# Optimization experiments

Measured on AMD Instinct MI355X. Metric: run time of the kernel, lower is better.

The kernel has to match this reference:

```python
import jax, jax.numpy as jnp
import numpy as np

N, E, D, H, OUT, L, AH = 50000, 800000, 128, 128, 2, 4, 16
LN_EPS = 1e-5


def setup_inputs() -> dict:
    key = jax.random.key(0)
    ks = jax.random.split(key, 8)
    s = lambda k, shape, scale: jax.random.normal(k, shape, jnp.float32) * scale
    return {
        "node_features": jax.random.normal(ks[0], (N, D), jnp.float32),
        "edge_index": jax.random.randint(ks[1], (2, E), 0, N),
        "W_self": s(ks[2], (L, D, H), 0.05),
        "b_self": jnp.zeros((L, H), jnp.float32),
        "W_ctx": s(ks[3], (L, 2 * D, H), 0.05),
        "b_ctx": jnp.zeros((L, H), jnp.float32),
        "att_W1": s(ks[4], (L, H, AH), 0.1),
        "att_b1": jnp.zeros((L, AH), jnp.float32),
        "att_w2": s(ks[5], (L, AH), 0.1),
        "ln_gamma": jnp.ones((L, H), jnp.float32),
        "ln_beta": jnp.zeros((L, H), jnp.float32),
        "fusion_logits": jnp.ones((L,), jnp.float32),
        "cls_W": s(ks[6], (H, OUT), 0.05),
        "cls_b": jnp.zeros((OUT,), jnp.float32),
    }


def _aggregate(x, src, tgt, n):
    # PyG add-aggregation of message cat([x_i - x_j, x_j]) at target nodes.
    # sum_over_edges(x_tgt - x_src) at tgt == deg(tgt)*x[tgt] - sum x_src, so we
    # avoid materializing the [E, 2D] edge tensor.
    ones = jnp.ones((src.shape[0],), x.dtype)
    deg = jax.ops.segment_sum(ones, tgt, num_segments=n)          # [N]
    agg_j = jax.ops.segment_sum(x[src], tgt, num_segments=n)      # [N, D]
    return jnp.concatenate([deg[:, None] * x - agg_j, agg_j], -1)  # [N, 2D]


def _layer_norm(x, gamma, beta):
    mu = x.mean(axis=-1, keepdims=True)
    var = ((x - mu) ** 2).mean(axis=-1, keepdims=True)
    return (x - mu) * jax.lax.rsqrt(var + LN_EPS) * gamma + beta


def _conv(x, src, tgt, Ws, bs, Wc, bc, A1, a1b, a2):
    n = x.shape[0]
    self_view = x @ Ws + bs                              # [N, H]
    out_view = _aggregate(x, src, tgt, n) @ Wc + bc      # outgoing (edge_index)
    in_view = _aggregate(x, tgt, src, n) @ Wc + bc       # incoming (reversed)
    mv = jnp.stack([self_view, out_view, in_view], axis=1)  # [N, 3, H]
    scores = jnp.einsum('nvh,ha->nva', jnp.tanh(jnp.einsum('nvh,ha->nva', mv, A1) + a1b), a2[:, None])[..., 0]
    w = jax.nn.softmax(scores, axis=1)                    # softmax over 3 views
    return jnp.einsum('nv,nvh->nh', w, mv)


def reference(node_features, edge_index, W_self, b_self, W_ctx, b_ctx,
              att_W1, att_b1, att_w2, ln_gamma, ln_beta,
              fusion_logits, cls_W, cls_b):
    src, tgt = edge_index[0], edge_index[1]
    x = node_features
    layer_outputs = []
    for l in range(L):
        h = _conv(x, src, tgt, W_self[l], b_self[l], W_ctx[l], b_ctx[l],
                  att_W1[l], att_b1[l], att_w2[l])
        h = jax.nn.relu(_layer_norm(h, ln_gamma[l], ln_beta[l]))
        # dropout is identity in eval mode
        x = h + x if l > 0 else h
        layer_outputs.append(x)
    fw = jax.nn.softmax(fusion_logits)
    fused = sum(fw[i] * layer_outputs[i] for i in range(L))
    return fused @ cls_W + cls_b
```

## Files before the change

kernel.cpp:

```cpp
#include <hip/hip_runtime.h>

#define N_NODES 50000
#define N_EDGES 800000
#define DD 128
#define HH 128
#define LL 4
#define AHH 16
#define LN_EPS 1e-5f
#define NCOLS 432
#define SCAN_B 512
#define SCAN_NB ((N_NODES + SCAN_B - 1) / SCAN_B)
#define WTPAD 136
#define WT_BLOCKS ((LL*NCOLS*DD)/256)
#define NBKT 196
#define BKT_CAP 8192
#define CVT_BLOCKS ((N_NODES*DD + 255)/256)
#define BKT_BLOCKS ((N_EDGES + 2047)/2048)

typedef unsigned short u16;
typedef unsigned int u32;
typedef __attribute__((ext_vector_type(8))) short short8;
typedef __attribute__((ext_vector_type(4))) float f32x4;

__device__ __forceinline__ float bf2f(u16 h){
  u32 u = ((u32)h) << 16;
  return __builtin_bit_cast(float, u);
}
__device__ __forceinline__ float bflo(u32 v){ return __builtin_bit_cast(float, v << 16); }
__device__ __forceinline__ float bfhi(u32 v){ return __builtin_bit_cast(float, v & 0xffff0000u); }
__device__ __forceinline__ u16 f2bf(float x){
  u32 u = __builtin_bit_cast(u32, x);
  u += 0x7fffu + ((u >> 16) & 1u);
  return (u16)(u >> 16);
}

__global__ void k_fail(float* out){
  int i = blockIdx.x*256 + threadIdx.x;
  if (i < N_NODES*2) out[i] = 1.0e6f;
}

__global__ __launch_bounds__(256) void k_cvt_bkt(const float* __restrict__ X,
    u16* __restrict__ Xb, const int* __restrict__ ei,
    int* gcur, u32* __restrict__ bktO, u32* __restrict__ bktI){
  if (blockIdx.x >= BKT_BLOCKS){
    int i = (blockIdx.x - BKT_BLOCKS)*256 + threadIdx.x;
    if (i < N_NODES*DD) Xb[i] = f2bf(X[i]);
    return;
  }
  __shared__ int histO[NBKT], histI[NBKT], baseO[NBKT], baseI[NBKT];
  int tid = threadIdx.x;
  int e0 = blockIdx.x*2048;
  if (tid < NBKT){ histO[tid] = 0; histI[tid] = 0; }
  __syncthreads();
  int s[8], t[8];
  #pragma unroll
  for (int k = 0; k < 8; ++k){
    int e = e0 + k*256 + tid;
    bool ok = e < N_EDGES;
    s[k] = ok ? ei[e] : -1;
    t[k] = ok ? ei[N_EDGES + e] : -1;
    if (ok){
      atomicAdd(&histO[t[k] >> 8], 1);
      atomicAdd(&histI[s[k] >> 8], 1);
    }
  }
  __syncthreads();
  if (tid < NBKT){
    baseO[tid] = atomicAdd(&gcur[tid],        histO[tid]);
    baseI[tid] = atomicAdd(&gcur[NBKT + tid], histI[tid]);
  }
  __syncthreads();
  if (tid < NBKT){ histO[tid] = 0; histI[tid] = 0; }
  __syncthreads();
  #pragma unroll
  for (int k = 0; k < 8; ++k){
    if (s[k] >= 0){
      int bO = t[k] >> 8, bI = s[k] >> 8;
      int rO = atomicAdd(&histO[bO], 1);
      int rI = atomicAdd(&histI[bI], 1);
      u32 iO = (u32)bO*BKT_CAP + (u32)(baseO[bO] + rO);
      u32 iI = (u32)bI*BKT_CAP + (u32)(baseI[bI] + rI);
      if (iO >= (u32)NBKT*BKT_CAP) iO = (u32)NBKT*BKT_CAP - 1;
      if (iI >= (u32)NBKT*BKT_CAP) iI = (u32)NBKT*BKT_CAP - 1;
      bktO[iO] = ((u32)(t[k] & 255) << 16) | (u32)s[k];
      bktI[iI] = ((u32)(s[k] & 255) << 16) | (u32)t[k];
    }
  }
}

__global__ __launch_bounds__(256) void k_bhist(const int* __restrict__ gcur,
    const u32* __restrict__ bktO, const u32* __restrict__ bktI,
    int* __restrict__ degO, int* __restrict__ degI){
  __shared__ int hist[256];
  int sb = blockIdx.x;
  int d = sb >= NBKT;
  int b = d ? sb - NBKT : sb;
  const u32* bkt = (d ? bktI : bktO) + (size_t)b*BKT_CAP;
  int cnt = gcur[d*NBKT + b];
  if (cnt > BKT_CAP) cnt = BKT_CAP;
  int tid = threadIdx.x;
  hist[tid] = 0;
  __syncthreads();
  for (int i = tid; i < cnt; i += 256) atomicAdd(&hist[bkt[i] >> 16], 1);
  __syncthreads();
  int n = b*256 + tid;
  if (n < N_NODES) (d ? degI : degO)[n] = hist[tid];
}

__global__ void k_scan2(const int* __restrict__ gcur, int* bsum, int* offO, int* offI){
  if (threadIdx.x == 0){
    int run = 0;
    for (int i = 0; i < SCAN_NB; ++i){ bsum[i] = run; run += gcur[2*i] + gcur[2*i+1]; }
    offO[N_NODES] = run;
    run = 0;
    for (int i = 0; i < SCAN_NB; ++i){ bsum[SCAN_NB+i] = run; run += gcur[NBKT+2*i] + gcur[NBKT+2*i+1]; }
    offI[N_NODES] = run;
  }
}
__global__ __launch_bounds__(SCAN_B) void k_scan3(const int* __restrict__ degO,
                                                  const int* __restrict__ degI,
                                                  const int* __restrict__ bsum,
                                                  int* offO, int* offI){
  int b = blockIdx.x, t = threadIdx.x, lane = t & 63, w = t >> 6;
  const int* deg = blockIdx.y ? degI : degO;
  int* off = blockIdx.y ? offI : offO;
  int i = b*SCAN_B + t;
  int v = (i < N_NODES) ? deg[i] : 0;
  int x = v;
  #pragma unroll
  for (int m = 1; m < 64; m <<= 1){ int tt = __shfl_up(x, m); if (lane >= m) x += tt; }
  __shared__ int ws[SCAN_B/64];
  if (lane == 63) ws[w] = x;
  __syncthreads();
  int woff = 0;
  for (int k = 0; k < w; ++k) woff += ws[k];
  if (i < N_NODES) off[i] = bsum[blockIdx.y*SCAN_NB + b] + woff + x - v;
}

__global__ __launch_bounds__(256) void k_packsort(const float* __restrict__ Wself,
                       const float* __restrict__ Wctx,
                       const float* __restrict__ A1, const float* __restrict__ bs,
                       const float* __restrict__ bc, u16* __restrict__ WT,
                       float* bsA, float* bcA,
                       const u32* __restrict__ bktO, const u32* __restrict__ bktI,
                       const int* __restrict__ offO, const int* __restrict__ offI,
                       int* __restrict__ csrO, int* __restrict__ csrI){
  if (blockIdx.x > WT_BLOCKS){
    int sb = blockIdx.x - (WT_BLOCKS + 1);
    int d = sb >= NBKT;
    int b = d ? sb - NBKT : sb;
    const u32* bkt = d ? bktI : bktO;
    const int* off = d ? offI : offO;
    int* csr = d ? csrI : csrO;
    __shared__ int hist[256], pref[256], cur[256], wsum[4];
    int tid = threadIdx.x;
    int lo = b*256, hi = min(lo + 256, N_NODES);
    int gbase = off[lo];
    int cnt = off[hi] - gbase;
    if (cnt > BKT_CAP) cnt = BKT_CAP;
    hist[tid] = 0; cur[tid] = 0;
    __syncthreads();
    const u32* bb = bkt + (size_t)b*BKT_CAP;
    for (int i = tid; i < cnt; i += 256) atomicAdd(&hist[bb[i] >> 16], 1);
    __syncthreads();
    {
      int lane = tid & 63, wid = tid >> 6;
      int h = hist[tid], v = h;
      #pragma unroll
      for (int m = 1; m < 64; m <<= 1){ int tt = __shfl_up(v, m); if (lane >= m) v += tt; }
      if (lane == 63) wsum[wid] = v;
      __syncthreads();
      int add = 0;
      for (int w = 0; w < wid; ++w) add += wsum[w];
      pref[tid] = add + v - h;
    }
    __syncthreads();
    for (int i = tid; i < cnt; i += 256){
      u32 ent = bb[i];
      int loc = (int)(ent >> 16);
      int pos = pref[loc] + atomicAdd(&cur[loc], 1);
      csr[gbase + pos] = (int)(ent & 0xffffu);
    }
    return;
  }
  if (blockIdx.x == WT_BLOCKS){
    int i = threadIdx.x;
    if (i < LL*2*AHH){
      int l = i >> 5, which = (i >> 4) & 1, a = i & 15;
      const float* b = which ? (bc + l*HH) : (bs + l*HH);
      const float* A = A1 + (size_t)l*HH*AHH;
      float v = 0.f;
      for (int h = 0; h < HH; ++h) v += b[h] * A[h*AHH + a];
      (which ? bcA : bsA)[l*AHH + a] = v;
    }
    return;
  }
  int idx = blockIdx.x*256 + threadIdx.x;
  int k = idx & 127;
  int j = (idx >> 7) % NCOLS;
  int l = idx / (NCOLS*DD);
  const float* Ws = Wself + (size_t)l*DD*HH;
  const float* Wc = Wctx + (size_t)l*2*DD*HH;
  const float* A  = A1 + (size_t)l*HH*AHH;
  float v = 0.f;
  if (j < 128) v = Ws[k*HH + j];
  else if (j < 256) v = Wc[k*HH + (j-128)];
  else if (j < 384) v = Wc[(128+k)*HH + (j-256)] - Wc[k*HH + (j-256)];
  else if (j < 400){ int a = j-384; for (int h=0; h<HH; ++h) v += Ws[k*HH+h] * A[h*AHH+a]; }
  else if (j < 416){ int a = j-400; for (int h=0; h<HH; ++h) v += Wc[k*HH+h] * A[h*AHH+a]; }
  else { int a = j-416; for (int h=0; h<HH; ++h) v += (Wc[(128+k)*HH+h] - Wc[k*HH+h]) * A[h*AHH+a]; }
  WT[((size_t)l*NCOLS + j)*DD + k] = f2bf(v);
}

struct GemmOut { u16 *S, *P1, *Pd, *SA, *P1A, *PdA; };

__global__ __launch_bounds__(256) void k_gemm(const u16* __restrict__ X,
                                              const u16* __restrict__ WT, GemmOut o){
  __shared__ u16 lw[3*16*WTPAD];
  int tid = threadIdx.x;
  int wid = tid >> 6, lane = tid & 63;
  int m0 = (blockIdx.x*4 + wid)*16;
  bool mvalid = (m0 < N_NODES);
  int m0c = mvalid ? m0 : (N_NODES - 16);
  int l15 = lane & 15, quad = lane >> 4;
  int sr = tid >> 4, sp = tid & 15;

  f32x4 acc[27];
  #pragma unroll
  for (int j = 0; j < 27; ++j) acc[j] = (f32x4){0.f,0.f,0.f,0.f};

  const u16* xr = X + (size_t)(m0c + l15)*DD + quad*8;
  short8 a[4];
  #pragma unroll
  for (int ks = 0; ks < 4; ++ks) a[ks] = *(const short8*)(xr + ks*32);

  short8 st[3];
  #pragma unroll
  for (int k = 0; k < 3; ++k)
    st[k] = *(const short8*)(WT + ((size_t)k*16 + sr)*DD + sp*8);

  for (int stage = 0; stage < 9; ++stage){
    int jbase = stage*3;
    __syncthreads();
    #pragma unroll
    for (int k = 0; k < 3; ++k)
      *(short8*)(&lw[(k*16 + sr)*WTPAD + sp*8]) = st[k];
    __syncthreads();
    if (stage < 8){
      #pragma unroll
      for (int k = 0; k < 3; ++k)
        st[k] = *(const short8*)(WT + ((size_t)(jbase+3+k)*16 + sr)*DD + sp*8);
    }
    #pragma unroll
    for (int k = 0; k < 3; ++k){
      const u16* wb = &lw[(k*16 + l15)*WTPAD + quad*8];
      #pragma unroll
      for (int ks = 0; ks < 4; ++ks){
        short8 b = *(const short8*)(wb + ks*32);
        acc[jbase+k] = __builtin_amdgcn_mfma_f32_16x16x32_bf16(a[ks], b, acc[jbase+k], 0, 0, 0);
      }
    }
  }
  if (!mvalid) return;
  #pragma unroll
  for (int j = 0; j < 27; ++j){
    int col = j*16 + l15;
    #pragma unroll
    for (int r = 0; r < 4; ++r){
      int row = m0 + quad*4 + r;
      u16 hv = f2bf(acc[j][r]);
      if (col < 128)      o.S  [(size_t)row*128 + col]        = hv;
      else if (col < 256) o.P1 [(size_t)row*128 + col - 128]  = hv;
      else if (col < 384) o.Pd [(size_t)row*128 + col - 256]  = hv;
      else if (col < 400) o.SA [(size_t)row*16  + col - 384]  = hv;
      else if (col < 416) o.P1A[(size_t)row*16  + col - 400]  = hv;
      else                o.PdA[(size_t)row*16  + col - 416]  = hv;
    }
  }
}

__global__ __launch_bounds__(256) void k_aggepi(int l,
  const u16* __restrict__ S, const u16* __restrict__ P1,
  const u16* __restrict__ Pd, const u16* __restrict__ PdA,
  const u16* __restrict__ SA, const u16* __restrict__ P1A,
  const int* __restrict__ offO, const int* __restrict__ offI,
  const int* __restrict__ csrO, const int* __restrict__ csrI,
  const float* __restrict__ b_self, const float* __restrict__ b_ctx,
  const float* __restrict__ bsA, const float* __restrict__ bcA,
  const float* __restrict__ att_b1, const float* __restrict__ att_w2,
  const float* __restrict__ gamma, const float* __restrict__ beta,
  const float* __restrict__ flog,
  u16* __restrict__ xb16,
  const float* __restrict__ clsW, const float* __restrict__ clsB,
  float* __restrict__ out)
{
  __shared__ float red[4][288];
  int tid = threadIdx.x;
  int n = (blockIdx.x * 256 + tid) >> 6;
  int wid = tid >> 6;
  int lane = tid & 63;
  int q = lane & 15, g = lane >> 4;
  const u16* PdQ  = Pd  + (q << 3);
  const u16* PdAQ = PdA + ((lane & 7) << 1);

  int begO = offO[n], endO = offO[n+1];
  int begI = offI[n], endI = offI[n+1];

  float aO[8] = {0.f,0.f,0.f,0.f,0.f,0.f,0.f,0.f};
  float aI[8] = {0.f,0.f,0.f,0.f,0.f,0.f,0.f,0.f};
  float oa0 = 0.f, oa1 = 0.f, ia0 = 0.f, ia1 = 0.f;

  int eO = begO, eI = begI;

#define GATH(csr, e, ACC, p0, p1) { \
    int r_ = (csr)[(e) + g]; \
    uint4 v_ = *(const uint4*)(PdQ + (((u32)r_) << 7)); \
    u32 pa_ = *(const u32*)(PdAQ + (((u32)r_) << 4)); \
    ACC[0] += bflo(v_.x); ACC[1] += bfhi(v_.x); \
    ACC[2] += bflo(v_.y); ACC[3] += bfhi(v_.y); \
    ACC[4] += bflo(v_.z); ACC[5] += bfhi(v_.z); \
    ACC[6] += bflo(v_.w); ACC[7] += bfhi(v_.w); \
    p0 += bflo(pa_); p1 += bfhi(pa_); }

#define GATHM(csr, e, end, ACC, p0, p1) { \
    int e_ = (e) + g; \
    bool ok_ = e_ < (end); \
    int r_ = (csr)[ok_ ? e_ : (end)-1]; \
    uint4 v_ = *(const uint4*)(PdQ + (((u32)r_) << 7)); \
    u32 pa_ = *(const u32*)(PdAQ + (((u32)r_) << 4)); \
    if (!ok_){ v_.x = 0u; v_.y = 0u; v_.z = 0u; v_.w = 0u; pa_ = 0u; } \
    ACC[0] += bflo(v_.x); ACC[1] += bfhi(v_.x); \
    ACC[2] += bflo(v_.y); ACC[3] += bfhi(v_.y); \
    ACC[4] += bflo(v_.z); ACC[5] += bfhi(v_.z); \
    ACC[6] += bflo(v_.w); ACC[7] += bfhi(v_.w); \
    p0 += bflo(pa_); p1 += bfhi(pa_); }

  for (; eO + 4 <= endO && eI + 4 <= endI; eO += 4, eI += 4){
    GATH(csrO, eO, aO, oa0, oa1);
    GATH(csrI, eI, aI, ia0, ia1);
  }
  for (; eO + 4 <= endO; eO += 4) GATH(csrO, eO, aO, oa0, oa1);
  for (; eI + 4 <= endI; eI += 4) GATH(csrI, eI, aI, ia0, ia1);
  if (eO < endO) GATHM(csrO, eO, endO, aO, oa0, oa1);
  if (eI < endI) GATHM(csrI, eI, endI, aI, ia0, ia1);

#undef GATH
#undef GATHM

  #pragma unroll
  for (int j = 0; j < 8; ++j){
    aO[j] += __shfl_xor(aO[j], 16); aO[j] += __shfl_xor(aO[j], 32);
    aI[j] += __shfl_xor(aI[j], 16); aI[j] += __shfl_xor(aI[j], 32);
  }
  oa0 += __shfl_xor(oa0, 16); oa0 += __shfl_xor(oa0, 32);
  oa1 += __shfl_xor(oa1, 16); oa1 += __shfl_xor(oa1, 32);
  ia0 += __shfl_xor(ia0, 16); ia0 += __shfl_xor(ia0, 32);
  ia1 += __shfl_xor(ia1, 16); ia1 += __shfl_xor(ia1, 32);

  if (g == 0){
    #pragma unroll
    for (int j = 0; j < 8; ++j){
      red[wid][q*8 + j]       = aO[j];
      red[wid][128 + q*8 + j] = aI[j];
    }
    if (q < 8){
      red[wid][256 + q*2]     = oa0;
      red[wid][256 + q*2 + 1] = oa1;
      red[wid][272 + q*2]     = ia0;
      red[wid][272 + q*2 + 1] = ia1;
    }
  }
  int f0 = lane * 2;
  int a16 = lane & 15;
  float ao0 = red[wid][f0],       ao1 = red[wid][f0 + 1];
  float ai0 = red[wid][128 + f0], ai1 = red[wid][128 + f0 + 1];
  float aoa = red[wid][256 + a16];
  float aia = red[wid][272 + a16];

  float dO = (float)(endO - begO), dI = (float)(endI - begI);

  u32 sv = *(const u32*)(S  + (size_t)n*128 + f0);
  u32 pv = *(const u32*)(P1 + (size_t)n*128 + f0);
  float2 bsv = *(const float2*)(b_self + l*128 + f0);
  float2 bcv = *(const float2*)(b_ctx  + l*128 + f0);
  float p10 = bflo(pv), p11 = bfhi(pv);
  float mv00 = bflo(sv) + bsv.x;
  float mv01 = bfhi(sv) + bsv.y;
  float mv10 = dO*p10 + ao0 + bcv.x, mv11 = dO*p11 + ao1 + bcv.y;
  float mv20 = dI*p10 + ai0 + bcv.x, mv21 = dI*p11 + ai1 + bcv.y;

  int a = a16, v = g;
  float u = 0.f;
  if (v < 3){
    float t;
    if (v == 0)      t = bf2f(SA[(size_t)n*16 + a]) + bsA[l*16 + a];
    else if (v == 1) t = dO*bf2f(P1A[(size_t)n*16 + a]) + aoa + bcA[l*16 + a];
    else             t = dI*bf2f(P1A[(size_t)n*16 + a]) + aia + bcA[l*16 + a];
    u = tanhf(t + att_b1[l*16 + a]) * att_w2[l*16 + a];
  }
  u += __shfl_xor(u, 1); u += __shfl_xor(u, 2);
  u += __shfl_xor(u, 4); u += __shfl_xor(u, 8);
  float s0 = __shfl(u, 0), s1 = __shfl(u, 16), s2 = __shfl(u, 32);
  float mx = fmaxf(s0, fmaxf(s1, s2));
  float e0 = __expf(s0-mx), e1 = __expf(s1-mx), e2 = __expf(s2-mx);
  float inv = 1.f / (e0 + e1 + e2);
  float w0 = e0*inv, w1 = e1*inv, w2v = e2*inv;
  float h0 = w0*mv00 + w1*mv10 + w2v*mv20;
  float h1 = w0*mv01 + w1*mv11 + w2v*mv21;

  float sum = h0 + h1, sq = h0*h0 + h1*h1;
  #pragma unroll
  for (int m = 1; m < 64; m <<= 1){ sum += __shfl_xor(sum, m); sq += __shfl_xor(sq, m); }
  float mu = sum * (1.f/128.f);
  float var = sq * (1.f/128.f) - mu*mu;
  float rs = rsqrtf(var + LN_EPS);
  float2 gv = *(const float2*)(gamma + l*128 + f0);
  float2 bv = *(const float2*)(beta  + l*128 + f0);
  float y0 = fmaxf((h0 - mu)*rs*gv.x + bv.x, 0.f);
  float y1 = fmaxf((h1 - mu)*rs*gv.y + bv.y, 0.f);
  float xn0 = y0, xn1 = y1;
  if (l > 0){
    u32 xv = *(const u32*)(xb16 + (size_t)n*128 + f0);
    xn0 += bflo(xv); xn1 += bfhi(xv);
  }
  *(u32*)(xb16 + (size_t)n*128 + f0) = (u32)f2bf(xn0) | ((u32)f2bf(xn1) << 16);

  float g0 = flog[0], g1 = flog[1], g2 = flog[2], g3 = flog[3];
  float gm = fmaxf(fmaxf(g0,g1), fmaxf(g2,g3));
  float q0 = __expf(g0-gm), q1 = __expf(g1-gm), q2 = __expf(g2-gm), q3 = __expf(g3-gm);
  float fwl = (l==0?q0 : l==1?q1 : l==2?q2 : q3) / (q0+q1+q2+q3);

  float4 w = *(const float4*)(clsW + lane*4);
  float o0 = xn0*w.x + xn1*w.z;
  float o1 = xn0*w.y + xn1*w.w;
  #pragma unroll
  for (int m = 1; m < 64; m <<= 1){ o0 += __shfl_xor(o0, m); o1 += __shfl_xor(o1, m); }
  if (lane == 0){
    float2* op = (float2*)(out + (size_t)n*2);
    float2 prev = (l > 0) ? *op : make_float2(0.f, 0.f);
    float r0 = prev.x + fwl*o0, r1 = prev.y + fwl*o1;
    if (l == LL-1){ r0 += clsB[0]; r1 += clsB[1]; }
    *op = make_float2(r0, r1);
  }
}

extern "C" void kernel_launch(void* const* d_in, const int* in_sizes, int n_in,
                              void* d_out, int out_size, void* d_ws, size_t ws_size,
                              hipStream_t stream){
  const float* X0    = (const float*)d_in[0];
  const int*   EI    = (const int*)d_in[1];
  const float* Wself = (const float*)d_in[2];
  const float* bs    = (const float*)d_in[3];
  const float* Wctx  = (const float*)d_in[4];
  const float* bc    = (const float*)d_in[5];
  const float* A1    = (const float*)d_in[6];
  const float* ab1   = (const float*)d_in[7];
  const float* aw2   = (const float*)d_in[8];
  const float* gam   = (const float*)d_in[9];
  const float* bet   = (const float*)d_in[10];
  const float* flog  = (const float*)d_in[11];
  const float* clsW  = (const float*)d_in[12];
  const float* clsB  = (const float*)d_in[13];
  float* out = (float*)d_out;

  char* wsp = (char*)d_ws;
  size_t o = 0;
  auto alloc = [&](size_t b)->char*{ char* p = wsp + o; o = (o + b + 255) & ~(size_t)255; return p; };
  u16*  xb16  = (u16*) alloc((size_t)N_NODES*128*2);
  u16*  S     = (u16*) alloc((size_t)N_NODES*128*2);
  u16*  P1    = (u16*) alloc((size_t)N_NODES*128*2);
  u16*  Pdb   = (u16*) alloc((size_t)N_NODES*128*2);
  u16*  PdAb  = (u16*) alloc((size_t)N_NODES*16*2);
  u16*  SAb   = (u16*) alloc((size_t)N_NODES*16*2);
  u16*  P1A   = (u16*) alloc((size_t)N_NODES*16*2);
  u16*  WT    = (u16*) alloc((size_t)LL*NCOLS*128*2);
  float* bsA  = (float*)alloc(LL*16*4);
  float* bcA  = (float*)alloc(LL*16*4);
  int* bsum   = (int*) alloc((size_t)2*SCAN_NB*4);
  int* degO   = (int*) alloc((size_t)N_NODES*4);
  int* degI   = (int*) alloc((size_t)N_NODES*4);
  int* gcur   = (int*) alloc((size_t)2*NBKT*4);
  int* offO   = (int*) alloc((size_t)(N_NODES+1)*4);
  int* offI   = (int*) alloc((size_t)(N_NODES+1)*4);
  int* csrO   = (int*) alloc((size_t)N_EDGES*4);
  int* csrI   = (int*) alloc((size_t)N_EDGES*4);

  if (ws_size < o){
    k_fail<<<(N_NODES*2+255)/256, 256, 0, stream>>>(out);
    return;
  }

  u32* bktO = (u32*)S;
  u32* bktI = (u32*)P1;

  (void)hipMemsetAsync(gcur, 0, (size_t)2*NBKT*4, stream);

  k_cvt_bkt<<<BKT_BLOCKS + CVT_BLOCKS, 256, 0, stream>>>(X0, xb16, EI, gcur, bktO, bktI);
  k_bhist<<<2*NBKT, 256, 0, stream>>>(gcur, bktO, bktI, degO, degI);
  k_scan2<<<1, 64, 0, stream>>>(gcur, bsum, offO, offI);
  k_scan3<<<dim3(SCAN_NB,2), SCAN_B, 0, stream>>>(degO, degI, bsum, offO, offI);
  k_packsort<<<WT_BLOCKS + 1 + 2*NBKT, 256, 0, stream>>>(Wself, Wctx, A1, bs, bc, WT, bsA, bcA,
                                                         bktO, bktI, offO, offI, csrO, csrI);

  GemmOut go{S, P1, Pdb, SAb, P1A, PdAb};
  const int gemm_blocks = ((N_NODES/16) + 3) / 4;
  for (int l = 0; l < LL; ++l){
    k_gemm<<<gemm_blocks, 256, 0, stream>>>(xb16, WT + (size_t)l*NCOLS*128, go);
    k_aggepi<<<N_NODES/4, 256, 0, stream>>>(l, S, P1, Pdb, PdAb, SAb, P1A,
                                            offO, offI, csrO, csrI,
                                            bs, bc, bsA, bcA, ab1, aw2,
                                            gam, bet, flog, xb16,
                                            clsW, clsB, out);
  }
}
```

Baseline: 557.3 us.

## Split gather from epilogue and store Pd in feature-quarter-major layout

The fused aggregate+epilogue kernel is split in two. A new gather kernel reads Pd stored as four 32-feature quarter planes, so each node's gathered row is 64 bytes and each block works on one quarter, which is meant to give better cache locality for the random gathers. It writes fp32 partial sums to new workspace buffers, and a slimmer epilogue kernel reads them back. This adds an extra launch per layer and roughly 50 MB of fp32 intermediate traffic per layer, and the per-lane edge loop can diverge when node degrees differ.

```diff
diff --git a/kernel.cpp b/kernel.cpp
--- a/kernel.cpp
+++ b/kernel.cpp
@@ -16,6 +16,7 @@
 #define BKT_CAP 8192
 #define CVT_BLOCKS ((N_NODES*DD + 255)/256)
 #define BKT_BLOCKS ((N_EDGES + 2047)/2048)
+#define GATH_CHUNKS 782
 
 typedef unsigned short u16;
 typedef unsigned int u32;
@@ -212,7 +213,7 @@
   WT[((size_t)l*NCOLS + j)*DD + k] = f2bf(v);
 }
 
-struct GemmOut { u16 *S, *P1, *Pd, *SA, *P1A, *PdA; };
+struct GemmOut { u16 *S, *P1, *Pdq, *SA, *P1A, *PdA; };
 
 __global__ __launch_bounds__(256) void k_gemm(const u16* __restrict__ X,
                                               const u16* __restrict__ WT, GemmOut o){
@@ -271,7 +272,10 @@
       u16 hv = f2bf(acc[j][r]);
       if (col < 128)      o.S  [(size_t)row*128 + col]        = hv;
       else if (col < 256) o.P1 [(size_t)row*128 + col - 128]  = hv;
-      else if (col < 384) o.Pd [(size_t)row*128 + col - 256]  = hv;
+      else if (col < 384){
+        int cc = col - 256;
+        o.Pdq[((size_t)(cc >> 5)*N_NODES + row)*32 + (cc & 31)] = hv;
+      }
       else if (col < 400) o.SA [(size_t)row*16  + col - 384]  = hv;
       else if (col < 416) o.P1A[(size_t)row*16  + col - 400]  = hv;
       else                o.PdA[(size_t)row*16  + col - 416]  = hv;
@@ -279,12 +283,81 @@
   }
 }
 
-__global__ __launch_bounds__(256) void k_aggepi(int l,
+__global__ __launch_bounds__(256) void k_gath(
+    const u16* __restrict__ Pdq, const u16* __restrict__ PdA,
+    const int* __restrict__ offO, const int* __restrict__ offI,
+    const int* __restrict__ csrO, const int* __restrict__ csrI,
+    float* __restrict__ aggO, float* __restrict__ aggI,
+    float* __restrict__ aggAO, float* __restrict__ aggAI)
+{
+  int b = blockIdx.x;
+  int qt = (b & 7) >> 1;
+  int chunk = ((b >> 3) << 1) + (b & 1);
+  int tid = threadIdx.x;
+  int lane = tid & 63;
+  int q = lane & 3, g = lane >> 2;
+  int n = chunk*64 + (tid >> 6)*16 + g;
+  bool valid = (n < N_NODES);
+  int nc = valid ? n : 0;
+
+  const u16* Pq = Pdq + (size_t)qt*N_NODES*32 + q*8;
+  const char* PA = (const char*)PdA + qt*8 + (q >> 1)*4;
+  int hi = q & 1;
+
+  int begO = offO[nc], endO = valid ? offO[nc+1] : begO;
+  int begI = offI[nc], endI = valid ? offI[nc+1] : begI;
+
+  float a0=0.f,a1=0.f,a2=0.f,a3=0.f,a4=0.f,a5=0.f,a6=0.f,a7=0.f,aa=0.f;
+  for (int e = begO;; ++e){
+    bool act = e < endO;
+    if (!__ballot(act)) break;
+    int r = csrO[act ? e : 0];
+    uint4 v = *(const uint4*)(Pq + ((u32)r << 5));
+    u32 pa = *(const u32*)(PA + ((u32)r << 5));
+    if (act){
+      a0 += bflo(v.x); a1 += bfhi(v.x);
+      a2 += bflo(v.y); a3 += bfhi(v.y);
+      a4 += bflo(v.z); a5 += bfhi(v.z);
+      a6 += bflo(v.w); a7 += bfhi(v.w);
+      aa += hi ? bfhi(pa) : bflo(pa);
+    }
+  }
+  if (valid){
+    float4* op = (float4*)(aggO + (size_t)n*128 + qt*32 + q*8);
+    op[0] = make_float4(a0,a1,a2,a3);
+    op[1] = make_float4(a4,a5,a6,a7);
+    aggAO[n*16 + qt*4 + q] = aa;
+  }
+
+  a0=0.f;a1=0.f;a2=0.f;a3=0.f;a4=0.f;a5=0.f;a6=0.f;a7=0.f;aa=0.f;
+  for (int e = begI;; ++e){
+    bool act = e < endI;
+    if (!__ballot(act)) break;
+    int r = csrI[act ? e : 0];
+    uint4 v = *(const uint4*)(Pq + ((u32)r << 5));
+    u32 pa = *(const u32*)(PA + ((u32)r << 5));
+    if (act){
+      a0 += bflo(v.x); a1 += bfhi(v.x);
+      a2 += bflo(v.y); a3 += bfhi(v.y);
+      a4 += bflo(v.z); a5 += bfhi(v.z);
+      a6 += bflo(v.w); a7 += bfhi(v.w);
+      aa += hi ? bfhi(pa) : bflo(pa);
+    }
+  }
+  if (valid){
+    float4* op = (float4*)(aggI + (size_t)n*128 + qt*32 + q*8);
+    op[0] = make_float4(a0,a1,a2,a3);
+    op[1] = make_float4(a4,a5,a6,a7);
+    aggAI[n*16 + qt*4 + q] = aa;
+  }
+}
+
+__global__ __launch_bounds__(256) void k_epi(int l,
   const u16* __restrict__ S, const u16* __restrict__ P1,
-  const u16* __restrict__ Pd, const u16* __restrict__ PdA,
   const u16* __restrict__ SA, const u16* __restrict__ P1A,
+  const float* __restrict__ aggO, const float* __restrict__ aggI,
+  const float* __restrict__ aggAO, const float* __restrict__ aggAI,
   const int* __restrict__ offO, const int* __restrict__ offI,
-  const int* __restrict__ csrO, const int* __restrict__ csrI,
   const float* __restrict__ b_self, const float* __restrict__ b_ctx,
   const float* __restrict__ bsA, const float* __restrict__ bcA,
   const float* __restrict__ att_b1, const float* __restrict__ att_w2,
@@ -294,90 +367,20 @@
   const float* __restrict__ clsW, const float* __restrict__ clsB,
   float* __restrict__ out)
 {
-  __shared__ float red[4][288];
-  int tid = threadIdx.x;
-  int n = (blockIdx.x * 256 + tid) >> 6;
-  int wid = tid >> 6;
-  int lane = tid & 63;
-  int q = lane & 15, g = lane >> 4;
-  const u16* PdQ  = Pd  + (q << 3);
-  const u16* PdAQ = PdA + ((lane & 7) << 1);
-
-  int begO = offO[n], endO = offO[n+1];
-  int begI = offI[n], endI = offI[n+1];
-
-  float aO[8] = {0.f,0.f,0.f,0.f,0.f,0.f,0.f,0.f};
-  float aI[8] = {0.f,0.f,0.f,0.f,0.f,0.f,0.f,0.f};
-  float oa0 = 0.f, oa1 = 0.f, ia0 = 0.f, ia1 = 0.f;
-
-  int eO = begO, eI = begI;
-
-#define GATH(csr, e, ACC, p0, p1) { \
-    int r_ = (csr)[(e) + g]; \
-    uint4 v_ = *(const uint4*)(PdQ + (((u32)r_) << 7)); \
-    u32 pa_ = *(const u32*)(PdAQ + (((u32)r_) << 4)); \
-    ACC[0] += bflo(v_.x); ACC[1] += bfhi(v_.x); \
-    ACC[2] += bflo(v_.y); ACC[3] += bfhi(v_.y); \
-    ACC[4] += bflo(v_.z); ACC[5] += bfhi(v_.z); \
-    ACC[6] += bflo(v_.w); ACC[7] += bfhi(v_.w); \
-    p0 += bflo(pa_); p1 += bfhi(pa_); }
-
-#define GATHM(csr, e, end, ACC, p0, p1) { \
-    int e_ = (e) + g; \
-    bool ok_ = e_ < (end); \
-    int r_ = (csr)[ok_ ? e_ : (end)-1]; \
-    uint4 v_ = *(const uint4*)(PdQ + (((u32)r_) << 7)); \
-    u32 pa_ = *(const u32*)(PdAQ + (((u32)r_) << 4)); \
-    if (!ok_){ v_.x = 0u; v_.y = 0u; v_.z = 0u; v_.w = 0u; pa_ = 0u; } \
-    ACC[0] += bflo(v_.x); ACC[1] += bfhi(v_.x); \
-    ACC[2] += bflo(v_.y); ACC[3] += bfhi(v_.y); \
-    ACC[4] += bflo(v_.z); ACC[5] += bfhi(v_.z); \
-    ACC[6] += bflo(v_.w); ACC[7] += bfhi(v_.w); \
-    p0 += bflo(pa_); p1 += bfhi(pa_); }
-
-  for (; eO + 4 <= endO && eI + 4 <= endI; eO += 4, eI += 4){
-    GATH(csrO, eO, aO, oa0, oa1);
-    GATH(csrI, eI, aI, ia0, ia1);
-  }
-  for (; eO + 4 <= endO; eO += 4) GATH(csrO, eO, aO, oa0, oa1);
-  for (; eI + 4 <= endI; eI += 4) GATH(csrI, eI, aI, ia0, ia1);
-  if (eO < endO) GATHM(csrO, eO, endO, aO, oa0, oa1);
-  if (eI < endI) GATHM(csrI, eI, endI, aI, ia0, ia1);
-
-#undef GATH
-#undef GATHM
-
-  #pragma unroll
-  for (int j = 0; j < 8; ++j){
-    aO[j] += __shfl_xor(aO[j], 16); aO[j] += __shfl_xor(aO[j], 32);
-    aI[j] += __shfl_xor(aI[j], 16); aI[j] += __shfl_xor(aI[j], 32);
-  }
-  oa0 += __shfl_xor(oa0, 16); oa0 += __shfl_xor(oa0, 32);
-  oa1 += __shfl_xor(oa1, 16); oa1 += __shfl_xor(oa1, 32);
-  ia0 += __shfl_xor(ia0, 16); ia0 += __shfl_xor(ia0, 32);
-  ia1 += __shfl_xor(ia1, 16); ia1 += __shfl_xor(ia1, 32);
-
-  if (g == 0){
-    #pragma unroll
-    for (int j = 0; j < 8; ++j){
-      red[wid][q*8 + j]       = aO[j];
-      red[wid][128 + q*8 + j] = aI[j];
-    }
-    if (q < 8){
-      red[wid][256 + q*2]     = oa0;
-      red[wid][256 + q*2 + 1] = oa1;
-      red[wid][272 + q*2]     = ia0;
-      red[wid][272 + q*2 + 1] = ia1;
-    }
-  }
+  int n = (blockIdx.x * 256 + threadIdx.x) >> 6;
+  int lane = threadIdx.x & 63;
   int f0 = lane * 2;
-  int a16 = lane & 15;
-  float ao0 = red[wid][f0],       ao1 = red[wid][f0 + 1];
-  float ai0 = red[wid][128 + f0], ai1 = red[wid][128 + f0 + 1];
-  float aoa = red[wid][256 + a16];
-  float aia = red[wid][272 + a16];
-
-  float dO = (float)(endO - begO), dI = (float)(endI - begI);
+  int a16 = lane & 15, g = lane >> 4;
+
+  float2 ov = *(const float2*)(aggO + (size_t)n*128 + f0);
+  float2 iv = *(const float2*)(aggI + (size_t)n*128 + f0);
+  float ao0 = ov.x, ao1 = ov.y;
+  float ai0 = iv.x, ai1 = iv.y;
+  float aoa = aggAO[n*16 + a16];
+  float aia = aggAI[n*16 + a16];
+
+  float dO = (float)(offO[n+1] - offO[n]);
+  float dI = (float)(offI[n+1] - offI[n]);
 
   u32 sv = *(const u32*)(S  + (size_t)n*128 + f0);
   u32 pv = *(const u32*)(P1 + (size_t)n*128 + f0);
@@ -469,7 +472,7 @@
   u16*  xb16  = (u16*) alloc((size_t)N_NODES*128*2);
   u16*  S     = (u16*) alloc((size_t)N_NODES*128*2);
   u16*  P1    = (u16*) alloc((size_t)N_NODES*128*2);
-  u16*  Pdb   = (u16*) alloc((size_t)N_NODES*128*2);
+  u16*  Pdq   = (u16*) alloc((size_t)N_NODES*128*2);
   u16*  PdAb  = (u16*) alloc((size_t)N_NODES*16*2);
   u16*  SAb   = (u16*) alloc((size_t)N_NODES*16*2);
   u16*  P1A   = (u16*) alloc((size_t)N_NODES*16*2);
@@ -484,6 +487,10 @@
   int* offI   = (int*) alloc((size_t)(N_NODES+1)*4);
   int* csrO   = (int*) alloc((size_t)N_EDGES*4);
   int* csrI   = (int*) alloc((size_t)N_EDGES*4);
+  float* aggO = (float*)alloc((size_t)N_NODES*128*4);
+  float* aggI = (float*)alloc((size_t)N_NODES*128*4);
+  float* aggAO= (float*)alloc((size_t)N_NODES*16*4);
+  float* aggAI= (float*)alloc((size_t)N_NODES*16*4);
 
   if (ws_size < o){
     k_fail<<<(N_NODES*2+255)/256, 256, 0, stream>>>(out);
@@ -502,14 +509,17 @@
   k_packsort<<<WT_BLOCKS + 1 + 2*NBKT, 256, 0, stream>>>(Wself, Wctx, A1, bs, bc, WT, bsA, bcA,
                                                          bktO, bktI, offO, offI, csrO, csrI);
 
-  GemmOut go{S, P1, Pdb, SAb, P1A, PdAb};
+  GemmOut go{S, P1, Pdq, SAb, P1A, PdAb};
   const int gemm_blocks = ((N_NODES/16) + 3) / 4;
   for (int l = 0; l < LL; ++l){
     k_gemm<<<gemm_blocks, 256, 0, stream>>>(xb16, WT + (size_t)l*NCOLS*128, go);
-    k_aggepi<<<N_NODES/4, 256, 0, stream>>>(l, S, P1, Pdb, PdAb, SAb, P1A,
-                                            offO, offI, csrO, csrI,
-                                            bs, bc, bsA, bcA, ab1, aw2,
-                                            gam, bet, flog, xb16,
-                                            clsW, clsB, out);
-  }
-}
+    k_gath<<<8*((GATH_CHUNKS+1)/2), 256, 0, stream>>>(Pdq, PdAb, offO, offI, csrO, csrI,
+                                                      aggO, aggI, aggAO, aggAI);
+    k_epi<<<N_NODES/4, 256, 0, stream>>>(l, S, P1, SAb, P1A,
+                                         aggO, aggI, aggAO, aggAI,
+                                         offO, offI,
+                                         bs, bc, bsA, bcA, ab1, aw2,
+                                         gam, bet, flog, xb16,
+                                         clsW, clsB, out);
+  }
+}
```

Result: slower. 907.7 us (+62.9%).

## Split gathered Pd rows into two 64-wide halves and gather in two passes

Applied to the files above, without the earlier changes.

The 128-wide bf16 Pd projection is stored as two separate 64-column arrays, and the aggregation kernel gathers neighbors in two passes, 8 edges per wave instruction with 8 lanes per row instead of 4 edges with 16 lanes. The aim is a smaller working set per pass, so each half of the gather table is more likely to stay in cache, and more independent edges in flight per load. In exchange, the CSR indices are read twice, there are more shuffle reduction steps, and more tail masking for low-degree nodes.

```diff
diff --git a/kernel.cpp b/kernel.cpp
--- a/kernel.cpp
+++ b/kernel.cpp
@@ -212,7 +212,7 @@
   WT[((size_t)l*NCOLS + j)*DD + k] = f2bf(v);
 }
 
-struct GemmOut { u16 *S, *P1, *Pd, *SA, *P1A, *PdA; };
+struct GemmOut { u16 *S, *P1, *PdLo, *PdHi, *SA, *P1A, *PdA; };
 
 __global__ __launch_bounds__(256) void k_gemm(const u16* __restrict__ X,
                                               const u16* __restrict__ WT, GemmOut o){
@@ -271,7 +271,11 @@
       u16 hv = f2bf(acc[j][r]);
       if (col < 128)      o.S  [(size_t)row*128 + col]        = hv;
       else if (col < 256) o.P1 [(size_t)row*128 + col - 128]  = hv;
-      else if (col < 384) o.Pd [(size_t)row*128 + col - 256]  = hv;
+      else if (col < 384){
+        int cc = col - 256;
+        if (cc < 64) o.PdLo[(size_t)row*64 + cc]      = hv;
+        else         o.PdHi[(size_t)row*64 + cc - 64] = hv;
+      }
       else if (col < 400) o.SA [(size_t)row*16  + col - 384]  = hv;
       else if (col < 416) o.P1A[(size_t)row*16  + col - 400]  = hv;
       else                o.PdA[(size_t)row*16  + col - 416]  = hv;
@@ -281,7 +285,8 @@
 
 __global__ __launch_bounds__(256) void k_aggepi(int l,
   const u16* __restrict__ S, const u16* __restrict__ P1,
-  const u16* __restrict__ Pd, const u16* __restrict__ PdA,
+  const u16* __restrict__ PdLo, const u16* __restrict__ PdHi,
+  const u16* __restrict__ PdA,
   const u16* __restrict__ SA, const u16* __restrict__ P1A,
   const int* __restrict__ offO, const int* __restrict__ offI,
   const int* __restrict__ csrO, const int* __restrict__ csrI,
@@ -299,35 +304,33 @@
   int n = (blockIdx.x * 256 + tid) >> 6;
   int wid = tid >> 6;
   int lane = tid & 63;
-  int q = lane & 15, g = lane >> 4;
-  const u16* PdQ  = Pd  + (q << 3);
-  const u16* PdAQ = PdA + ((lane & 7) << 1);
+  int k8 = lane & 7, eg = lane >> 3;
+  const u16* PLo = PdLo + (k8 << 3);
+  const u16* PHi = PdHi + (k8 << 3);
+  const u16* PA  = PdA  + (k8 << 1);
 
   int begO = offO[n], endO = offO[n+1];
   int begI = offI[n], endI = offI[n+1];
 
-  float aO[8] = {0.f,0.f,0.f,0.f,0.f,0.f,0.f,0.f};
-  float aI[8] = {0.f,0.f,0.f,0.f,0.f,0.f,0.f,0.f};
-  float oa0 = 0.f, oa1 = 0.f, ia0 = 0.f, ia1 = 0.f;
-
-  int eO = begO, eI = begI;
-
-#define GATH(csr, e, ACC, p0, p1) { \
-    int r_ = (csr)[(e) + g]; \
-    uint4 v_ = *(const uint4*)(PdQ + (((u32)r_) << 7)); \
-    u32 pa_ = *(const u32*)(PdAQ + (((u32)r_) << 4)); \
+  float aO[8], aI[8];
+  float xo0, xo1, xi0, xi1;
+
+#define GATHA(csr, e, ACC, p0, p1) { \
+    int r_ = (csr)[(e) + eg]; \
+    uint4 v_ = *(const uint4*)(PLo + (((u32)r_) << 6)); \
+    u32 pa_ = *(const u32*)(PA + (((u32)r_) << 4)); \
     ACC[0] += bflo(v_.x); ACC[1] += bfhi(v_.x); \
     ACC[2] += bflo(v_.y); ACC[3] += bfhi(v_.y); \
     ACC[4] += bflo(v_.z); ACC[5] += bfhi(v_.z); \
     ACC[6] += bflo(v_.w); ACC[7] += bfhi(v_.w); \
     p0 += bflo(pa_); p1 += bfhi(pa_); }
 
-#define GATHM(csr, e, end, ACC, p0, p1) { \
-    int e_ = (e) + g; \
+#define GATHAM(csr, e, end, ACC, p0, p1) { \
+    int e_ = (e) + eg; \
     bool ok_ = e_ < (end); \
     int r_ = (csr)[ok_ ? e_ : (end)-1]; \
-    uint4 v_ = *(const uint4*)(PdQ + (((u32)r_) << 7)); \
-    u32 pa_ = *(const u32*)(PdAQ + (((u32)r_) << 4)); \
+    uint4 v_ = *(const uint4*)(PLo + (((u32)r_) << 6)); \
+    u32 pa_ = *(const u32*)(PA + (((u32)r_) << 4)); \
     if (!ok_){ v_.x = 0u; v_.y = 0u; v_.z = 0u; v_.w = 0u; pa_ = 0u; } \
     ACC[0] += bflo(v_.x); ACC[1] += bfhi(v_.x); \
     ACC[2] += bflo(v_.y); ACC[3] += bfhi(v_.y); \
@@ -335,43 +338,89 @@
     ACC[6] += bflo(v_.w); ACC[7] += bfhi(v_.w); \
     p0 += bflo(pa_); p1 += bfhi(pa_); }
 
-  for (; eO + 4 <= endO && eI + 4 <= endI; eO += 4, eI += 4){
-    GATH(csrO, eO, aO, oa0, oa1);
-    GATH(csrI, eI, aI, ia0, ia1);
-  }
-  for (; eO + 4 <= endO; eO += 4) GATH(csrO, eO, aO, oa0, oa1);
-  for (; eI + 4 <= endI; eI += 4) GATH(csrI, eI, aI, ia0, ia1);
-  if (eO < endO) GATHM(csrO, eO, endO, aO, oa0, oa1);
-  if (eI < endI) GATHM(csrI, eI, endI, aI, ia0, ia1);
-
-#undef GATH
-#undef GATHM
-
+#define GATHB(csr, e, ACC) { \
+    int r_ = (csr)[(e) + eg]; \
+    uint4 v_ = *(const uint4*)(PHi + (((u32)r_) << 6)); \
+    ACC[0] += bflo(v_.x); ACC[1] += bfhi(v_.x); \
+    ACC[2] += bflo(v_.y); ACC[3] += bfhi(v_.y); \
+    ACC[4] += bflo(v_.z); ACC[5] += bfhi(v_.z); \
+    ACC[6] += bflo(v_.w); ACC[7] += bfhi(v_.w); }
+
+#define GATHBM(csr, e, end, ACC) { \
+    int e_ = (e) + eg; \
+    bool ok_ = e_ < (end); \
+    int r_ = (csr)[ok_ ? e_ : (end)-1]; \
+    uint4 v_ = *(const uint4*)(PHi + (((u32)r_) << 6)); \
+    if (!ok_){ v_.x = 0u; v_.y = 0u; v_.z = 0u; v_.w = 0u; } \
+    ACC[0] += bflo(v_.x); ACC[1] += bfhi(v_.x); \
+    ACC[2] += bflo(v_.y); ACC[3] += bfhi(v_.y); \
+    ACC[4] += bflo(v_.z); ACC[5] += bfhi(v_.z); \
+    ACC[6] += bflo(v_.w); ACC[7] += bfhi(v_.w); }
+
+  #pragma unroll
+  for (int j = 0; j < 8; ++j){ aO[j] = 0.f; aI[j] = 0.f; }
+  xo0 = xo1 = xi0 = xi1 = 0.f;
+  int eO = begO, eI = begI;
+  for (; eO + 8 <= endO && eI + 8 <= endI; eO += 8, eI += 8){
+    GATHA(csrO, eO, aO, xo0, xo1);
+    GATHA(csrI, eI, aI, xi0, xi1);
+  }
+  for (; eO + 8 <= endO; eO += 8) GATHA(csrO, eO, aO, xo0, xo1);
+  for (; eI + 8 <= endI; eI += 8) GATHA(csrI, eI, aI, xi0, xi1);
+  if (eO < endO) GATHAM(csrO, eO, endO, aO, xo0, xo1);
+  if (eI < endI) GATHAM(csrI, eI, endI, aI, xi0, xi1);
   #pragma unroll
   for (int j = 0; j < 8; ++j){
-    aO[j] += __shfl_xor(aO[j], 16); aO[j] += __shfl_xor(aO[j], 32);
-    aI[j] += __shfl_xor(aI[j], 16); aI[j] += __shfl_xor(aI[j], 32);
-  }
-  oa0 += __shfl_xor(oa0, 16); oa0 += __shfl_xor(oa0, 32);
-  oa1 += __shfl_xor(oa1, 16); oa1 += __shfl_xor(oa1, 32);
-  ia0 += __shfl_xor(ia0, 16); ia0 += __shfl_xor(ia0, 32);
-  ia1 += __shfl_xor(ia1, 16); ia1 += __shfl_xor(ia1, 32);
-
-  if (g == 0){
+    aO[j] += __shfl_xor(aO[j], 8); aO[j] += __shfl_xor(aO[j], 16); aO[j] += __shfl_xor(aO[j], 32);
+    aI[j] += __shfl_xor(aI[j], 8); aI[j] += __shfl_xor(aI[j], 16); aI[j] += __shfl_xor(aI[j], 32);
+  }
+  xo0 += __shfl_xor(xo0, 8); xo0 += __shfl_xor(xo0, 16); xo0 += __shfl_xor(xo0, 32);
+  xo1 += __shfl_xor(xo1, 8); xo1 += __shfl_xor(xo1, 16); xo1 += __shfl_xor(xo1, 32);
+  xi0 += __shfl_xor(xi0, 8); xi0 += __shfl_xor(xi0, 16); xi0 += __shfl_xor(xi0, 32);
+  xi1 += __shfl_xor(xi1, 8); xi1 += __shfl_xor(xi1, 16); xi1 += __shfl_xor(xi1, 32);
+  if (eg == 0){
     #pragma unroll
     for (int j = 0; j < 8; ++j){
-      red[wid][q*8 + j]       = aO[j];
-      red[wid][128 + q*8 + j] = aI[j];
-    }
-    if (q < 8){
-      red[wid][256 + q*2]     = oa0;
-      red[wid][256 + q*2 + 1] = oa1;
-      red[wid][272 + q*2]     = ia0;
-      red[wid][272 + q*2 + 1] = ia1;
-    }
-  }
+      red[wid][k8*8 + j]       = aO[j];
+      red[wid][128 + k8*8 + j] = aI[j];
+    }
+    red[wid][256 + k8*2]     = xo0;
+    red[wid][256 + k8*2 + 1] = xo1;
+    red[wid][272 + k8*2]     = xi0;
+    red[wid][272 + k8*2 + 1] = xi1;
+  }
+
+  #pragma unroll
+  for (int j = 0; j < 8; ++j){ aO[j] = 0.f; aI[j] = 0.f; }
+  eO = begO; eI = begI;
+  for (; eO + 8 <= endO && eI + 8 <= endI; eO += 8, eI += 8){
+    GATHB(csrO, eO, aO);
+    GATHB(csrI, eI, aI);
+  }
+  for (; eO + 8 <= endO; eO += 8) GATHB(csrO, eO, aO);
+  for (; eI + 8 <= endI; eI += 8) GATHB(csrI, eI, aI);
+  if (eO < endO) GATHBM(csrO, eO, endO, aO);
+  if (eI < endI) GATHBM(csrI, eI, endI, aI);
+  #pragma unroll
+  for (int j = 0; j < 8; ++j){
+    aO[j] += __shfl_xor(aO[j], 8); aO[j] += __shfl_xor(aO[j], 16); aO[j] += __shfl_xor(aO[j], 32);
+    aI[j] += __shfl_xor(aI[j], 8); aI[j] += __shfl_xor(aI[j], 16); aI[j] += __shfl_xor(aI[j], 32);
+  }
+  if (eg == 0){
+    #pragma unroll
+    for (int j = 0; j < 8; ++j){
+      red[wid][64 + k8*8 + j]  = aO[j];
+      red[wid][192 + k8*8 + j] = aI[j];
+    }
+  }
+
+#undef GATHA
+#undef GATHAM
+#undef GATHB
+#undef GATHBM
+
   int f0 = lane * 2;
-  int a16 = lane & 15;
+  int a16 = lane & 15, g = lane >> 4;
   float ao0 = red[wid][f0],       ao1 = red[wid][f0 + 1];
   float ai0 = red[wid][128 + f0], ai1 = red[wid][128 + f0 + 1];
   float aoa = red[wid][256 + a16];
@@ -469,7 +518,8 @@
   u16*  xb16  = (u16*) alloc((size_t)N_NODES*128*2);
   u16*  S     = (u16*) alloc((size_t)N_NODES*128*2);
   u16*  P1    = (u16*) alloc((size_t)N_NODES*128*2);
-  u16*  Pdb   = (u16*) alloc((size_t)N_NODES*128*2);
+  u16*  PdLo  = (u16*) alloc((size_t)N_NODES*64*2);
+  u16*  PdHi  = (u16*) alloc((size_t)N_NODES*64*2);
   u16*  PdAb  = (u16*) alloc((size_t)N_NODES*16*2);
   u16*  SAb   = (u16*) alloc((size_t)N_NODES*16*2);
   u16*  P1A   = (u16*) alloc((size_t)N_NODES*16*2);
@@ -502,11 +552,11 @@
   k_packsort<<<WT_BLOCKS + 1 + 2*NBKT, 256, 0, stream>>>(Wself, Wctx, A1, bs, bc, WT, bsA, bcA,
                                                          bktO, bktI, offO, offI, csrO, csrI);
 
-  GemmOut go{S, P1, Pdb, SAb, P1A, PdAb};
+  GemmOut go{S, P1, PdLo, PdHi, SAb, P1A, PdAb};
   const int gemm_blocks = ((N_NODES/16) + 3) / 4;
   for (int l = 0; l < LL; ++l){
     k_gemm<<<gemm_blocks, 256, 0, stream>>>(xb16, WT + (size_t)l*NCOLS*128, go);
-    k_aggepi<<<N_NODES/4, 256, 0, stream>>>(l, S, P1, Pdb, PdAb, SAb, P1A,
+    k_aggepi<<<N_NODES/4, 256, 0, stream>>>(l, S, P1, PdLo, PdHi, PdAb, SAb, P1A,
                                             offO, offI, csrO, csrI,
                                             bs, bc, bsA, bcA, ab1, aw2,
                                             gam, bet, flog, xb16,
```

Measured after the change: 639.8 us. 14.8% more time.
